# Performance work log

Hardware: AMD Instinct MI355X
Metric: run time of the kernel (lower is better)

## Reference

```python
import jax, jax.numpy as jnp
import numpy as np

B = 16384
MV = 512   # movie_vector_size
UV = 512   # user_vector_size
NM = 16    # num_dense_movie_embeddings
NU = 16    # num_dense_user_embeddings
DS = 16    # dense_embedding_size
MLP = [256, 128, 1]


def setup_inputs() -> dict:
    key = jax.random.key(0)
    ks = jax.random.split(key, 12)
    inp = {
        'movie_vectors': jax.random.normal(ks[0], (B, MV), jnp.float32),
        'user_vectors': jax.random.normal(ks[1], (B, UV), jnp.float32),
        # embedding towers: Linear(in, DS*N + 1), stored as [in, out]
        'Wm': jax.random.normal(ks[2], (MV, DS * NM + 1), jnp.float32) * (1.0 / np.sqrt(MV)),
        'bm': jax.random.normal(ks[3], (DS * NM + 1,), jnp.float32) * 0.01,
        'Wu': jax.random.normal(ks[4], (UV, DS * NU + 1), jnp.float32) * (1.0 / np.sqrt(UV)),
        'bu': jax.random.normal(ks[5], (DS * NU + 1,), jnp.float32) * 0.01,
    }
    d_in = (NM + NU) * DS  # 512
    dims = [d_in] + MLP
    for i in range(len(MLP)):
        inp[f'W{i+1}'] = jax.random.normal(ks[6 + 2*i], (dims[i], dims[i+1]), jnp.float32) * (1.0 / np.sqrt(dims[i]))
        inp[f'b{i+1}'] = jax.random.normal(ks[7 + 2*i], (dims[i+1],), jnp.float32) * 0.01
    return inp


def reference(movie_vectors, user_vectors, Wm, bm, Wu, bu, W1, b1, W2, b2, W3, b3):
    batch = movie_vectors.shape[0]
    movie_dense = movie_vectors @ Wm + bm          # [B, DS*NM+1]
    user_dense = user_vectors @ Wu + bu            # [B, DS*NU+1]
    fm_additive = movie_dense[:, -1] + user_dense[:, -1]            # [B]
    m_split = movie_dense[:, :-1].reshape(batch, NM, DS)            # [B, NM, DS]
    u_split = user_dense[:, :-1].reshape(batch, NU, DS)             # [B, NU, DS]
    fm_interactions = jnp.einsum('bik,bjk->bij', m_split, u_split).reshape(batch, -1)  # [B, NM*NU]
    all_dense = jnp.concatenate([movie_dense[:, :-1], user_dense[:, :-1]], axis=-1)    # [B, (NM+NU)*DS]
    h = jax.nn.relu(all_dense @ W1 + b1)
    h = jax.nn.relu(h @ W2 + b2)
    mlp_out = h @ W3 + b3                                           # [B, 1]
    logit = mlp_out + fm_additive[:, None] + jnp.sum(fm_interactions, axis=-1, keepdims=True)
    return logit
```

## Files before the change

### kernel.cpp

```cpp
#include <hip/hip_runtime.h>


#define NTH 512
#define RB  32

typedef __bf16 bf16x8 __attribute__((ext_vector_type(8)));
typedef float  f32x4  __attribute__((ext_vector_type(4)));
typedef unsigned short u16x8 __attribute__((ext_vector_type(8)));

#define WS_WMF  0
#define WS_WUF  294912
#define WS_W1F  589824
#define WS_W2F  851968
#define WS_BIAS 917504

#define BPITCH   1040
#define L_BST    0
#define L_DENSE  33280
#define L_OUT    66048
#define LDSB     66176

__device__ __forceinline__ unsigned short f2bf(float f) {
  unsigned u = __builtin_bit_cast(unsigned, f);
  u += 0x7FFFu + ((u >> 16) & 1u);
  return (unsigned short)(u >> 16);
}

__device__ __forceinline__ f32x4 mfma_bf16(bf16x8 a, bf16x8 b, f32x4 c) {
  return __builtin_amdgcn_mfma_f32_16x16x32_bf16(a, b, c, 0, 0, 0);
}

extern "C" __global__ __launch_bounds__(64) void deepfm_prep(
    const float* __restrict__ Wm, const float* __restrict__ bm,
    const float* __restrict__ Wu, const float* __restrict__ bu,
    const float* __restrict__ W1, const float* __restrict__ W2,
    const float* __restrict__ b3, char* __restrict__ ws) {
  const int bid = blockIdx.x;
  const int l = threadIdx.x;
  const int fi = l & 15, q = l >> 4;
  unsigned short h[8];
  if (bid < 576) {
    const int t = bid / 288, rem = bid % 288;
    const int kg = rem / 18, ft = rem % 18;
    const float* W = t ? Wu : Wm;
    char* outp = ws + (t ? WS_WUF : WS_WMF);
    const int f = ft * 16 + fi;
#pragma unroll
    for (int e = 0; e < 8; ++e) {
      const int k = kg * 32 + q * 8 + e;
      float val;
      if (f < 256) val = W[k * 257 + f];
      else if (f < 272) {
        float s = 0.f;
#pragma unroll
        for (int i = 0; i < 16; ++i) s += W[k * 257 + i * 16 + (f - 256)];
        val = s;
      } else if (f == 272) val = W[k * 257 + 256];
      else val = 0.f;
      h[e] = f2bf(val);
    }
    uint4 o;
    o.x = h[0] | ((unsigned)h[1] << 16); o.y = h[2] | ((unsigned)h[3] << 16);
    o.z = h[4] | ((unsigned)h[5] << 16); o.w = h[6] | ((unsigned)h[7] << 16);
    *(uint4*)(outp + (((kg * 18 + ft) * 64 + l) << 4)) = o;
  } else if (bid < 832) {
    const int bb = bid - 576;
    const int kg = bb / 16, ft = bb % 16;
    const int f = ft * 16 + fi;
#pragma unroll
    for (int e = 0; e < 8; ++e) h[e] = f2bf(W1[(kg * 32 + q * 8 + e) * 256 + f]);
    uint4 o;
    o.x = h[0] | ((unsigned)h[1] << 16); o.y = h[2] | ((unsigned)h[3] << 16);
    o.z = h[4] | ((unsigned)h[5] << 16); o.w = h[6] | ((unsigned)h[7] << 16);
    *(uint4*)(ws + WS_W1F + (((kg * 16 + ft) * 64 + l) << 4)) = o;
  } else if (bid < 896) {
    const int bb = bid - 832;
    const int kg = bb / 8, ft = bb % 8;
    const int f = ft * 16 + fi;
#pragma unroll
    for (int e = 0; e < 8; ++e) h[e] = f2bf(W2[(kg * 32 + q * 8 + e) * 128 + f]);
    uint4 o;
    o.x = h[0] | ((unsigned)h[1] << 16); o.y = h[2] | ((unsigned)h[3] << 16);
    o.z = h[4] | ((unsigned)h[5] << 16); o.w = h[6] | ((unsigned)h[7] << 16);
    *(uint4*)(ws + WS_W2F + (((kg * 8 + ft) * 64 + l) << 4)) = o;
  } else {
    float* aux = (float*)(ws + WS_BIAS);
    if (l < 16) {
      float s = 0.f;
      for (int i = 0; i < 16; ++i) s += bm[i * 16 + l];
      aux[l] = s;
    } else if (l < 32) {
      const int k = l - 16;
      float s = 0.f;
      for (int i = 0; i < 16; ++i) s += bu[i * 16 + k];
      aux[l] = s;
    } else if (l == 32) {
      aux[32] = bm[256] + bu[256] + b3[0];
    }
  }
}

extern "C" __global__ __launch_bounds__(NTH, 4) void deepfm_main(
    const float* __restrict__ movie, const float* __restrict__ user,
    const float* __restrict__ bm, const float* __restrict__ bu,
    const float* __restrict__ b1, const float* __restrict__ b2,
    const float* __restrict__ W3, const char* __restrict__ ws,
    float* __restrict__ out) {
  extern __shared__ __align__(16) char lds[];
  char* const bstage    = lds + L_BST;
  char* const densefrag = lds + L_DENSE;
  char* const h1frag    = lds + L_BST;
  float* const outpart  = (float*)(lds + L_OUT);

  const int tid = threadIdx.x;
  const int w   = tid >> 6;
  const int l   = tid & 63;
  const int cn  = l & 15;
  const int q   = l >> 4;
  const int row0 = blockIdx.x * RB;

  const int axi  = (w >> 2) & 1;
  const int axrt = w & 1;

  if (tid < 32) outpart[tid] = 0.f;

  const f32x4 zz = {0.f, 0.f, 0.f, 0.f};
  f32x4 accM = zz, accU = zz;
  f32x4 a00, a01, a10, a11;
  const float* auxb = (const float*)(ws + WS_BIAS);

#pragma unroll
  for (int t = 0; t < 2; ++t) {
    const float* inp = t ? user : movie;
    const char* WF = ws + (t ? WS_WUF : WS_WMF);

    if (t) __syncthreads();
#pragma unroll
    for (int p = 0; p < 8; ++p) {
      const int idx = p * 512 + tid;
      const int r = idx >> 7, f4 = idx & 127;
      const int k0 = f4 * 4;
      const float4 v = *(const float4*)(inp + (size_t)(row0 + r) * 512 + k0);
      uint2 o;
      o.x = f2bf(v.x) | ((unsigned)f2bf(v.y) << 16);
      o.y = f2bf(v.z) | ((unsigned)f2bf(v.w) << 16);
      *(uint2*)(bstage + r * BPITCH + k0 * 2) = o;
    }
    __syncthreads();

    a00 = zz; a01 = zz; a10 = zz; a11 = zz;
    f32x4 axc = zz;
#pragma unroll 4
    for (int kg = 0; kg < 16; ++kg) {
      const bf16x8 bf0 = *(const bf16x8*)(bstage + cn * BPITCH + kg * 64 + q * 16);
      const bf16x8 bf1 = *(const bf16x8*)(bstage + (16 + cn) * BPITCH + kg * 64 + q * 16);
      const bf16x8 a0 = *(const bf16x8*)(WF + (((kg * 18 + w) * 64 + l) << 4));
      const bf16x8 a1 = *(const bf16x8*)(WF + (((kg * 18 + w + 8) * 64 + l) << 4));
      const bf16x8 ax = *(const bf16x8*)(WF + (((kg * 18 + 16 + axi) * 64 + l) << 4));
      a00 = mfma_bf16(a0, bf0, a00);
      a01 = mfma_bf16(a0, bf1, a01);
      a10 = mfma_bf16(a1, bf0, a10);
      a11 = mfma_bf16(a1, bf1, a11);
      axc = mfma_bf16(ax, axrt ? bf1 : bf0, axc);
    }
    if (t == 0) accM = axc; else accU = axc;

    const float* bt = t ? bu : bm;
    const f32x4 accA[2][2] = {{a00, a01}, {a10, a11}};
#pragma unroll
    for (int s = 0; s < 2; ++s) {
      const int ft = w + s * 8;
      const int fb = ft * 16 + q * 4;
      const float g0 = bt[fb], g1 = bt[fb + 1], g2 = bt[fb + 2], g3 = bt[fb + 3];
      const int kd = t * 256 + fb;
      const int kgd = kd >> 5, qd = (kd >> 3) & 3, ed = kd & 4;
#pragma unroll
      for (int rt = 0; rt < 2; ++rt) {
        const f32x4 v = accA[s][rt];
        uint2 p;
        p.x = f2bf(v[0] + g0) | ((unsigned)f2bf(v[1] + g1) << 16);
        p.y = f2bf(v[2] + g2) | ((unsigned)f2bf(v[3] + g3) << 16);
        *(uint2*)(densefrag + (((kgd * 2 + rt) * 64 + qd * 16 + cn) << 4) +
                  (ed ? 8 : 0)) = p;
      }
    }
  }

  __syncthreads();

  if (w < 2) {
    float p = 0.f;
#pragma unroll
    for (int reg = 0; reg < 4; ++reg) {
      const float msv = accM[reg] + auxb[q * 4 + reg];
      const float usv = accU[reg] + auxb[16 + q * 4 + reg];
      p += msv * usv;
    }
    p += __shfl_xor(p, 16, 64);
    p += __shfl_xor(p, 32, 64);
    if (l < 16) atomicAdd(&outpart[w * 16 + cn], p);
  } else if ((w == 4 || w == 5) && q == 0) {
    atomicAdd(&outpart[(w - 4) * 16 + cn], accM[0] + accU[0] + auxb[32]);
  }

  a00 = zz; a01 = zz; a10 = zz; a11 = zz;
  {
    const char* W1F = ws + WS_W1F;
#pragma unroll 4
    for (int kg = 0; kg < 16; ++kg) {
      const bf16x8 b0  = *(const bf16x8*)(densefrag + (((kg * 2 + 0) * 64 + l) << 4));
      const bf16x8 b1f = *(const bf16x8*)(densefrag + (((kg * 2 + 1) * 64 + l) << 4));
      const bf16x8 a0 = *(const bf16x8*)(W1F + (((kg * 16 + w) * 64 + l) << 4));
      const bf16x8 a1 = *(const bf16x8*)(W1F + (((kg * 16 + w + 8) * 64 + l) << 4));
      a00 = mfma_bf16(a0, b0,  a00);
      a01 = mfma_bf16(a0, b1f, a01);
      a10 = mfma_bf16(a1, b0,  a10);
      a11 = mfma_bf16(a1, b1f, a11);
    }
    const f32x4 accA[2][2] = {{a00, a01}, {a10, a11}};
#pragma unroll
    for (int s = 0; s < 2; ++s) {
      const int ft = w + s * 8;
      const int fb = ft * 16 + q * 4;
      const float g0 = b1[fb], g1 = b1[fb + 1], g2 = b1[fb + 2], g3 = b1[fb + 3];
      const int kgd = fb >> 5, qd = (fb >> 3) & 3, ed = fb & 4;
#pragma unroll
      for (int rt = 0; rt < 2; ++rt) {
        const f32x4 v = accA[s][rt];
        uint2 p;
        p.x = f2bf(fmaxf(v[0] + g0, 0.f)) | ((unsigned)f2bf(fmaxf(v[1] + g1, 0.f)) << 16);
        p.y = f2bf(fmaxf(v[2] + g2, 0.f)) | ((unsigned)f2bf(fmaxf(v[3] + g3, 0.f)) << 16);
        *(uint2*)(h1frag + (((kgd * 2 + rt) * 64 + qd * 16 + cn) << 4) +
                  (ed ? 8 : 0)) = p;
      }
    }
  }

  __syncthreads();

  {
    const char* W2F = ws + WS_W2F;
    f32x4 d0 = zz, d1 = zz;
#pragma unroll 4
    for (int kg = 0; kg < 8; ++kg) {
      const bf16x8 b0  = *(const bf16x8*)(h1frag + (((kg * 2 + 0) * 64 + l) << 4));
      const bf16x8 b1f = *(const bf16x8*)(h1frag + (((kg * 2 + 1) * 64 + l) << 4));
      const bf16x8 a0 = *(const bf16x8*)(W2F + (((kg * 8 + w) * 64 + l) << 4));
      d0 = mfma_bf16(a0, b0,  d0);
      d1 = mfma_bf16(a0, b1f, d1);
    }
    const int fb = w * 16 + q * 4;
    float bb[4], ww[4];
#pragma unroll
    for (int i = 0; i < 4; ++i) { bb[i] = b2[fb + i]; ww[i] = W3[fb + i]; }
    const f32x4 acc3[2] = {d0, d1};
#pragma unroll
    for (int rt = 0; rt < 2; ++rt) {
      float p = 0.f;
#pragma unroll
      for (int reg = 0; reg < 4; ++reg)
        p += fmaxf(acc3[rt][reg] + bb[reg], 0.f) * ww[reg];
      p += __shfl_xor(p, 16, 64);
      p += __shfl_xor(p, 32, 64);
      if (l < 16) atomicAdd(&outpart[rt * 16 + cn], p);
    }
  }

  __syncthreads();
  if (tid < 32) out[row0 + tid] = outpart[tid];
}

extern "C" void kernel_launch(void* const* d_in, const int* in_sizes, int n_in,
                              void* d_out, int out_size, void* d_ws, size_t ws_size,
                              hipStream_t stream) {
  const float* movie = (const float*)d_in[0];
  const float* user  = (const float*)d_in[1];
  const float* Wm = (const float*)d_in[2];
  const float* bm = (const float*)d_in[3];
  const float* Wu = (const float*)d_in[4];
  const float* bu = (const float*)d_in[5];
  const float* W1 = (const float*)d_in[6];
  const float* b1 = (const float*)d_in[7];
  const float* W2 = (const float*)d_in[8];
  const float* b2 = (const float*)d_in[9];
  const float* W3 = (const float*)d_in[10];
  const float* b3 = (const float*)d_in[11];
  char* ws = (char*)d_ws;
  float* out = (float*)d_out;

  (void)hipFuncSetAttribute((const void*)deepfm_main,
                            hipFuncAttributeMaxDynamicSharedMemorySize, LDSB);

  deepfm_prep<<<897, 64, 0, stream>>>(Wm, bm, Wu, bu, W1, W2, b3, ws);
  deepfm_main<<<512, NTH, LDSB, stream>>>(movie, user, bm, bu, b1, b2, W3, ws, out);
}
```

Baseline: 138.4 us.

## Run movie and user towers concurrently across wave halves with K-split staging

After: 136.4 us. About the same (-1.4%).

```diff
diff --git a/kernel.cpp b/kernel.cpp
--- a/kernel.cpp
+++ b/kernel.cpp
@@ -6,7 +6,6 @@
 
 typedef __bf16 bf16x8 __attribute__((ext_vector_type(8)));
 typedef float  f32x4  __attribute__((ext_vector_type(4)));
-typedef unsigned short u16x8 __attribute__((ext_vector_type(8)));
 
 #define WS_WMF  0
 #define WS_WUF  294912
@@ -14,11 +13,13 @@
 #define WS_W2F  851968
 #define WS_BIAS 917504
 
-#define BPITCH   1040
-#define L_BST    0
-#define L_DENSE  33280
-#define L_OUT    66048
-#define LDSB     66176
+#define BPITCH  528
+#define L_BST   0
+#define L_DENSE 33792
+#define L_FM    66560
+#define L_ADD   70912
+#define L_OUT   71168
+#define LDSB    71296
 
 __device__ __forceinline__ unsigned short f2bf(float f) {
   unsigned u = __builtin_bit_cast(unsigned, f);
@@ -30,17 +31,18 @@
   return __builtin_amdgcn_mfma_f32_16x16x32_bf16(a, b, c, 0, 0, 0);
 }
 
-extern "C" __global__ __launch_bounds__(64) void deepfm_prep(
+extern "C" __global__ __launch_bounds__(256) void deepfm_prep(
     const float* __restrict__ Wm, const float* __restrict__ bm,
     const float* __restrict__ Wu, const float* __restrict__ bu,
     const float* __restrict__ W1, const float* __restrict__ W2,
     const float* __restrict__ b3, char* __restrict__ ws) {
-  const int bid = blockIdx.x;
-  const int l = threadIdx.x;
+  const int unit = blockIdx.x * 4 + (threadIdx.x >> 6);
+  if (unit >= 897) return;
+  const int l = threadIdx.x & 63;
   const int fi = l & 15, q = l >> 4;
   unsigned short h[8];
-  if (bid < 576) {
-    const int t = bid / 288, rem = bid % 288;
+  if (unit < 576) {
+    const int t = unit / 288, rem = unit % 288;
     const int kg = rem / 18, ft = rem % 18;
     const float* W = t ? Wu : Wm;
     char* outp = ws + (t ? WS_WUF : WS_WMF);
@@ -63,8 +65,8 @@
     o.x = h[0] | ((unsigned)h[1] << 16); o.y = h[2] | ((unsigned)h[3] << 16);
     o.z = h[4] | ((unsigned)h[5] << 16); o.w = h[6] | ((unsigned)h[7] << 16);
     *(uint4*)(outp + (((kg * 18 + ft) * 64 + l) << 4)) = o;
-  } else if (bid < 832) {
-    const int bb = bid - 576;
+  } else if (unit < 832) {
+    const int bb = unit - 576;
     const int kg = bb / 16, ft = bb % 16;
     const int f = ft * 16 + fi;
 #pragma unroll
@@ -73,8 +75,8 @@
     o.x = h[0] | ((unsigned)h[1] << 16); o.y = h[2] | ((unsigned)h[3] << 16);
     o.z = h[4] | ((unsigned)h[5] << 16); o.w = h[6] | ((unsigned)h[7] << 16);
     *(uint4*)(ws + WS_W1F + (((kg * 16 + ft) * 64 + l) << 4)) = o;
-  } else if (bid < 896) {
-    const int bb = bid - 832;
+  } else if (unit < 896) {
+    const int bb = unit - 832;
     const int kg = bb / 8, ft = bb % 8;
     const int f = ft * 16 + fi;
 #pragma unroll
@@ -110,6 +112,8 @@
   char* const bstage    = lds + L_BST;
   char* const densefrag = lds + L_DENSE;
   char* const h1frag    = lds + L_BST;
+  float* const fmbuf    = (float*)(lds + L_FM);
+  float* const addbuf   = (float*)(lds + L_ADD);
   float* const outpart  = (float*)(lds + L_OUT);
 
   const int tid = threadIdx.x;
@@ -119,60 +123,63 @@
   const int q   = l >> 4;
   const int row0 = blockIdx.x * RB;
 
-  const int axi  = (w >> 2) & 1;
-  const int axrt = w & 1;
-
-  if (tid < 32) outpart[tid] = 0.f;
+  const int tw   = w >> 2;
+  const int wi   = w & 3;
+  const int axi  = wi & 1;
+  const int axrt = wi >> 1;
 
   const f32x4 zz = {0.f, 0.f, 0.f, 0.f};
-  f32x4 accM = zz, accU = zz;
-  f32x4 a00, a01, a10, a11;
   const float* auxb = (const float*)(ws + WS_BIAS);
 
-#pragma unroll
-  for (int t = 0; t < 2; ++t) {
-    const float* inp = t ? user : movie;
-    const char* WF = ws + (t ? WS_WUF : WS_WMF);
-
-    if (t) __syncthreads();
-#pragma unroll
-    for (int p = 0; p < 8; ++p) {
-      const int idx = p * 512 + tid;
-      const int r = idx >> 7, f4 = idx & 127;
-      const int k0 = f4 * 4;
-      const float4 v = *(const float4*)(inp + (size_t)(row0 + r) * 512 + k0);
-      uint2 o;
-      o.x = f2bf(v.x) | ((unsigned)f2bf(v.y) << 16);
-      o.y = f2bf(v.z) | ((unsigned)f2bf(v.w) << 16);
-      *(uint2*)(bstage + r * BPITCH + k0 * 2) = o;
-    }
-    __syncthreads();
-
-    a00 = zz; a01 = zz; a10 = zz; a11 = zz;
+  {
+    const char* WF = ws + (tw ? WS_WUF : WS_WMF);
+    const char* brow = bstage + tw * 32 * BPITCH;
+    f32x4 a0r0 = zz, a0r1 = zz, a1r0 = zz, a1r1 = zz;
+    f32x4 a2r0 = zz, a2r1 = zz, a3r0 = zz, a3r1 = zz;
     f32x4 axc = zz;
-#pragma unroll 4
-    for (int kg = 0; kg < 16; ++kg) {
-      const bf16x8 bf0 = *(const bf16x8*)(bstage + cn * BPITCH + kg * 64 + q * 16);
-      const bf16x8 bf1 = *(const bf16x8*)(bstage + (16 + cn) * BPITCH + kg * 64 + q * 16);
-      const bf16x8 a0 = *(const bf16x8*)(WF + (((kg * 18 + w) * 64 + l) << 4));
-      const bf16x8 a1 = *(const bf16x8*)(WF + (((kg * 18 + w + 8) * 64 + l) << 4));
-      const bf16x8 ax = *(const bf16x8*)(WF + (((kg * 18 + 16 + axi) * 64 + l) << 4));
-      a00 = mfma_bf16(a0, bf0, a00);
-      a01 = mfma_bf16(a0, bf1, a01);
-      a10 = mfma_bf16(a1, bf0, a10);
-      a11 = mfma_bf16(a1, bf1, a11);
-      axc = mfma_bf16(ax, axrt ? bf1 : bf0, axc);
-    }
-    if (t == 0) accM = axc; else accU = axc;
-
-    const float* bt = t ? bu : bm;
-    const f32x4 accA[2][2] = {{a00, a01}, {a10, a11}};
-#pragma unroll
-    for (int s = 0; s < 2; ++s) {
-      const int ft = w + s * 8;
+
+    for (int h = 0; h < 2; ++h) {
+      if (h) __syncthreads();
+#pragma unroll
+      for (int p = 0; p < 8; ++p) {
+        const int idx = p * 512 + tid;
+        const int r = idx >> 6, f4 = idx & 63;
+        const float* src = (r >= 32) ? user : movie;
+        const float4 v = *(const float4*)(src + (size_t)(row0 + (r & 31)) * 512 +
+                                          h * 256 + f4 * 4);
+        uint2 o;
+        o.x = f2bf(v.x) | ((unsigned)f2bf(v.y) << 16);
+        o.y = f2bf(v.z) | ((unsigned)f2bf(v.w) << 16);
+        *(uint2*)(bstage + r * BPITCH + f4 * 8) = o;
+      }
+      __syncthreads();
+
+#pragma unroll 2
+      for (int kgl = 0; kgl < 8; ++kgl) {
+        const int kg = h * 8 + kgl;
+        const bf16x8 bf0 = *(const bf16x8*)(brow + cn * BPITCH + kgl * 64 + q * 16);
+        const bf16x8 bf1 = *(const bf16x8*)(brow + (16 + cn) * BPITCH + kgl * 64 + q * 16);
+        const bf16x8 A0 = *(const bf16x8*)(WF + (((kg * 18 + wi * 4 + 0) * 64 + l) << 4));
+        const bf16x8 A1 = *(const bf16x8*)(WF + (((kg * 18 + wi * 4 + 1) * 64 + l) << 4));
+        const bf16x8 A2 = *(const bf16x8*)(WF + (((kg * 18 + wi * 4 + 2) * 64 + l) << 4));
+        const bf16x8 A3 = *(const bf16x8*)(WF + (((kg * 18 + wi * 4 + 3) * 64 + l) << 4));
+        const bf16x8 AX = *(const bf16x8*)(WF + (((kg * 18 + 16 + axi) * 64 + l) << 4));
+        a0r0 = mfma_bf16(A0, bf0, a0r0);  a0r1 = mfma_bf16(A0, bf1, a0r1);
+        a1r0 = mfma_bf16(A1, bf0, a1r0);  a1r1 = mfma_bf16(A1, bf1, a1r1);
+        a2r0 = mfma_bf16(A2, bf0, a2r0);  a2r1 = mfma_bf16(A2, bf1, a2r1);
+        a3r0 = mfma_bf16(A3, bf0, a3r0);  a3r1 = mfma_bf16(A3, bf1, a3r1);
+        axc  = mfma_bf16(AX, axrt ? bf1 : bf0, axc);
+      }
+    }
+
+    const float* bt = tw ? bu : bm;
+    const f32x4 accA[4][2] = {{a0r0, a0r1}, {a1r0, a1r1}, {a2r0, a2r1}, {a3r0, a3r1}};
+#pragma unroll
+    for (int s = 0; s < 4; ++s) {
+      const int ft = wi * 4 + s;
       const int fb = ft * 16 + q * 4;
       const float g0 = bt[fb], g1 = bt[fb + 1], g2 = bt[fb + 2], g3 = bt[fb + 3];
-      const int kd = t * 256 + fb;
+      const int kd = tw * 256 + fb;
       const int kgd = kd >> 5, qd = (kd >> 3) & 3, ed = kd & 4;
 #pragma unroll
       for (int rt = 0; rt < 2; ++rt) {
@@ -184,28 +191,30 @@
                   (ed ? 8 : 0)) = p;
       }
     }
+
+    if (axi == 0) {
+#pragma unroll
+      for (int reg = 0; reg < 4; ++reg)
+        fmbuf[(tw * 32 + axrt * 16 + cn) * 17 + (q * 4 + reg)] = axc[reg];
+    } else if (q == 0) {
+      addbuf[tw * 32 + axrt * 16 + cn] = axc[0];
+    }
   }
 
   __syncthreads();
 
-  if (w < 2) {
+  if (tid < 32) {
     float p = 0.f;
 #pragma unroll
-    for (int reg = 0; reg < 4; ++reg) {
-      const float msv = accM[reg] + auxb[q * 4 + reg];
-      const float usv = accU[reg] + auxb[16 + q * 4 + reg];
-      p += msv * usv;
-    }
-    p += __shfl_xor(p, 16, 64);
-    p += __shfl_xor(p, 32, 64);
-    if (l < 16) atomicAdd(&outpart[w * 16 + cn], p);
-  } else if ((w == 4 || w == 5) && q == 0) {
-    atomicAdd(&outpart[(w - 4) * 16 + cn], accM[0] + accU[0] + auxb[32]);
-  }
-
-  a00 = zz; a01 = zz; a10 = zz; a11 = zz;
+    for (int k = 0; k < 16; ++k)
+      p += (fmbuf[tid * 17 + k] + auxb[k]) *
+           (fmbuf[(32 + tid) * 17 + k] + auxb[16 + k]);
+    outpart[tid] = p + addbuf[tid] + addbuf[32 + tid] + auxb[32];
+  }
+
   {
     const char* W1F = ws + WS_W1F;
+    f32x4 a00 = zz, a01 = zz, a10 = zz, a11 = zz;
 #pragma unroll 4
     for (int kg = 0; kg < 16; ++kg) {
       const bf16x8 b0  = *(const bf16x8*)(densefrag + (((kg * 2 + 0) * 64 + l) << 4));
@@ -291,6 +300,6 @@
   (void)hipFuncSetAttribute((const void*)deepfm_main,
                             hipFuncAttributeMaxDynamicSharedMemorySize, LDSB);
 
-  deepfm_prep<<<897, 64, 0, stream>>>(Wm, bm, Wu, bu, W1, W2, b3, ws);
+  deepfm_prep<<<225, 256, 0, stream>>>(Wm, bm, Wu, bu, W1, W2, b3, ws);
   deepfm_main<<<512, NTH, LDSB, stream>>>(movie, user, bm, bu, b1, b2, W3, ws, out);
 }
```
